# Performance work log

Measured on AMD Instinct MI355X. Metric: run time of the kernel, lower is better.

Reference implementation:

```python
import jax, jax.numpy as jnp
import numpy as np

B, G = 256, 24
N = B * G
D_IN, HEADS, D_HEAD = 128, 8, 64  # out_channels = in_channels//2 = 64, concat=False
EFF = HEADS * D_HEAD
EPS = 1e-5
SCALE = float(np.sqrt(D_HEAD))

def _gelu(x):
    return jax.nn.gelu(x, approximate=False)

def _pff(x, w1, b1, w2, b2):
    # PositionwiseFeedForward, dropout=0 (eval)
    return _gelu(x @ w1.T + b1) @ w2.T + b2

def _graph_norm_global(x, w, b, ms):
    # GraphNorm called without batch -> single graph over all N nodes
    mean = jnp.mean(x, axis=0, keepdims=True)
    out = x - mean * ms
    var = jnp.mean(out * out, axis=0, keepdims=True)
    return w * out / jnp.sqrt(var + EPS) + b

def _graph_norm(x, w, b, ms, batch, nseg):
    cnt = jax.ops.segment_sum(jnp.ones((x.shape[0],), x.dtype), batch, nseg)[:, None]
    mean = jax.ops.segment_sum(x, batch, nseg) / cnt
    out = x - mean[batch] * ms
    var = jax.ops.segment_sum(out * out, batch, nseg) / cnt
    return w * out / jnp.sqrt(var + EPS)[batch] + b

def _segment_softmax(logits, seg, nseg):
    m = jax.ops.segment_max(logits, seg, num_segments=nseg)
    e = jnp.exp(logits - m[seg])
    s = jax.ops.segment_sum(e, seg, num_segments=nseg)
    return e / (s[seg] + 1e-16)

def _attn_conv(x, edge_index, p):
    (nq_w, nq_b, nq_ms, wq, bq, wk, bk, wv, bv,
     no_w, no_b, no_ms, o_w1, o_b1, o_w2, o_b2) = p
    n = x.shape[0]
    xin = x
    xn = _graph_norm_global(x, nq_w, nq_b, nq_ms)
    q = (xn @ wq.T + bq).reshape(n, HEADS, D_HEAD)
    k = (xn @ wk.T + bk).reshape(n, HEADS, D_HEAD)
    v = (xn @ wv.T + bv).reshape(n, HEADS, D_HEAD)
    loops = jnp.arange(n, dtype=edge_index.dtype)  # add_self_loops appends
    src = jnp.concatenate([edge_index[0], loops])
    dst = jnp.concatenate([edge_index[1], loops])
    qk = jnp.sum(q[dst] * k[src], axis=-1) / SCALE          # [E', H]
    alpha = _segment_softmax(qk, dst, n)                     # segment softmax over dst
    aggr = jax.ops.segment_sum(v[src] * alpha[:, :, None], dst, num_segments=n)  # [N,H,Dh]
    aggr = aggr.mean(axis=1)                                 # concat=False: head mean -> [N,64]
    init = xin.reshape(n, D_IN // D_HEAD, D_HEAD).sum(axis=1)  # sum-fold 128 -> 64 residual
    h = aggr + init
    hn = _graph_norm_global(h, no_w, no_b, no_ms)
    return h + _pff(hn, o_w1, o_b1, o_w2, o_b2)


def setup_inputs() -> dict:
    key = jax.random.key(0)
    ks = jax.random.split(key, 12)
    # block-dense edges: fully connected within each set, no self loops
    a = np.arange(G)
    ii, jj = np.meshgrid(a, a, indexing='ij')
    m = ii != jj
    dst_l, src_l = ii[m], jj[m]
    offs = (np.arange(B) * G)[:, None]
    src = (src_l[None, :] + offs).reshape(-1)
    dst = (dst_l[None, :] + offs).reshape(-1)
    edge_index = jnp.asarray(np.stack([src, dst]), dtype=jnp.int64)
    batch = jnp.asarray(np.repeat(np.arange(B), G), dtype=jnp.int64)
    ptr = jnp.asarray(np.arange(B + 1) * G, dtype=jnp.int64)
    x = jax.random.normal(ks[0], (N, D_IN), jnp.float32)
    def lin(k, o, i):
        return jax.random.normal(k, (o, i), jnp.float32) * (1.0 / np.sqrt(i))
    d = dict(x=x, edge_index=edge_index, ptr=ptr, batch=batch)
    d.update(nq_w=jnp.ones((D_IN,)), nq_b=jnp.zeros((D_IN,)), nq_ms=jnp.ones((D_IN,)))
    d.update(wq=lin(ks[1], EFF, D_IN), bq=jnp.zeros((EFF,)),
             wk=lin(ks[2], EFF, D_IN), bk=jnp.zeros((EFF,)),
             wv=lin(ks[3], EFF, D_IN), bv=jnp.zeros((EFF,)))
    d.update(no_w=jnp.ones((D_HEAD,)), no_b=jnp.zeros((D_HEAD,)), no_ms=jnp.ones((D_HEAD,)))
    d.update(o_w1=lin(ks[4], D_HEAD, D_HEAD), o_b1=jnp.zeros((D_HEAD,)),
             o_w2=lin(ks[5], D_HEAD, D_HEAD), o_b2=jnp.zeros((D_HEAD,)))
    d.update(pn_w=jnp.ones((D_HEAD,)), pn_b=jnp.zeros((D_HEAD,)), pn_ms=jnp.ones((D_HEAD,)))
    d.update(p_w1=lin(ks[6], D_HEAD, D_HEAD), p_b1=jnp.zeros((D_HEAD,)),
             p_w2=lin(ks[7], 1, D_HEAD), p_b2=jnp.zeros((1,)))
    return d


def reference(x, edge_index, ptr, batch,
              nq_w, nq_b, nq_ms, wq, bq, wk, bk, wv, bv,
              no_w, no_b, no_ms, o_w1, o_b1, o_w2, o_b2,
              pn_w, pn_b, pn_ms, p_w1, p_b1, p_w2, p_b2):
    nseg = ptr.shape[0] - 1
    h = _attn_conv(x, edge_index,
                   (nq_w, nq_b, nq_ms, wq, bq, wk, bk, wv, bv,
                    no_w, no_b, no_ms, o_w1, o_b1, o_w2, o_b2))   # [N,64]
    hn = _graph_norm(h, pn_w, pn_b, pn_ms, batch, nseg)
    score = _pff(hn, p_w1, p_b1, p_w2, p_b2)                       # [N,1]
    w = _segment_softmax(score[:, 0], batch, nseg)[:, None]        # per-set softmax
    return jax.ops.segment_sum(x * w, batch, num_segments=nseg)    # [B, 128]
```

## Files before the change

kernel.cpp:

```cpp
#include <hip/hip_runtime.h>
#include <stdint.h>


#define N_NODES 6144
#define GSIZE 24
#define NGRAPH 256
#define DIN 128
#define DH 64
#define EFF 512
#define EPSN 1e-5f

typedef __attribute__((ext_vector_type(8))) __bf16 bf16x8;
typedef __attribute__((ext_vector_type(4))) float f32x4;
union U16B { uint4 u; bf16x8 v; unsigned short s[8]; };

__device__ inline unsigned short f2bf(float f){
  unsigned u = __float_as_uint(f);
  u += 0x7fff + ((u>>16)&1);
  return (unsigned short)(u>>16);
}
__device__ inline float gelu_exact(float x){ return 0.5f*x*(1.0f+erff(x*0.70710678118654752f)); }

#define XS    0
#define HS    256
#define HCF   384
#define WT1   393600
#define WT2   397696
#define PWT1  401792
#define FBo   405888
#define WCVT_BYTE  1703936

#define QS3 260

__global__ __launch_bounds__(256)
void k_pre(const float* __restrict__ x,
           const float* __restrict__ o_w1, const float* __restrict__ o_w2,
           const float* __restrict__ p_w1,
           const float* __restrict__ o_b1, const float* __restrict__ o_b2,
           const float* __restrict__ p_b1, const float* __restrict__ p_w2,
           const float* __restrict__ p_b2,
           const float* __restrict__ wq, const float* __restrict__ wk,
           const float* __restrict__ wv,
           float* __restrict__ wsf){
  int t = threadIdx.x;
  int bi = blockIdx.x;
  if(bi < 192){
    int c = t & 127, h = t >> 7;
    float s = 0.f, q = 0.f;
    #pragma unroll
    for(int r = 0; r < 16; ++r){
      float v = x[(size_t)(bi*32 + h + 2*r)*DIN + c];
      s += v; q += v*v;
    }
    __shared__ float sm[256], sm2[256];
    sm[t] = s; sm2[t] = q;
    __syncthreads();
    if(t < 128){
      atomicAdd(&wsf[XS + t],       sm[t] + sm[t+128]);
      atomicAdd(&wsf[XS + 128 + t], sm2[t] + sm2[t+128]);
    }
    return;
  }
  if(bi < 195){
    const float* src; float* dst;
    if(bi == 192){ src = o_w1; dst = wsf + WT1; }
    else if(bi == 193){ src = o_w2; dst = wsf + WT2; }
    else { src = p_w1; dst = wsf + PWT1; }
    for(int p = t; p < DH*DH; p += 256){
      int r = p >> 6, c = p & 63;
      dst[c*DH + r] = src[p];
    }
    if(bi == 192){
      float* fb = wsf + FBo;
      if(t < 64){
        fb[t]       = o_b1[t];
        fb[64 + t]  = o_b2[t];
        fb[128 + t] = p_b1[t];
        fb[192 + t] = p_w2[t];
      }
      if(t == 0) fb[256] = p_b2[0];
    }
    return;
  }
  int j = bi - 195;
  int mat = j >> 2, seg = j & 3;
  const float* src = (mat==0) ? wq : (mat==1) ? wk : wv;
  unsigned short* dst = (unsigned short*)((char*)wsf + WCVT_BYTE)
                        + (size_t)mat*EFF*DIN + seg*16384;
  const float* sp = src + seg*16384;
  for(int e = t*8; e < 16384; e += 2048){
    float4 a = *(const float4*)(sp + e);
    float4 b = *(const float4*)(sp + e + 4);
    U16B o;
    o.s[0]=f2bf(a.x); o.s[1]=f2bf(a.y); o.s[2]=f2bf(a.z); o.s[3]=f2bf(a.w);
    o.s[4]=f2bf(b.x); o.s[5]=f2bf(b.y); o.s[6]=f2bf(b.z); o.s[7]=f2bf(b.w);
    *(uint4*)(dst + e) = o.u;
  }
}

#define LOADW3(nt, W, B) do{ \
  const int mat_ = (nt)>>2, sub_ = (nt)&3; \
  const unsigned short* wp_ = wcvt + (size_t)mat_*EFF*DIN \
      + (size_t)(gh*64 + sub_*16 + m)*DIN + lq*8; \
  W[0] = *(const uint4*)(wp_);      W[1] = *(const uint4*)(wp_ + 32); \
  W[2] = *(const uint4*)(wp_ + 64); W[3] = *(const uint4*)(wp_ + 96); \
  const float* bias_ = (mat_==0) ? bq : (mat_==1) ? bk : bv; \
  B = *(const float4*)(bias_ + gh*64 + sub_*16 + lq*4); \
}while(0)

#define COMPW3(nt, W, B) do{ \
  const int mat_ = (nt)>>2, sub_ = (nt)&3; \
  f32x4 a0_ = {0.f,0.f,0.f,0.f}, a1_ = {0.f,0.f,0.f,0.f}; \
  U16B w8_; \
  w8_.u = W[0]; \
  a0_ = __builtin_amdgcn_mfma_f32_16x16x32_bf16(w8_.v, afr[0][0], a0_, 0, 0, 0); \
  a1_ = __builtin_amdgcn_mfma_f32_16x16x32_bf16(w8_.v, afr[1][0], a1_, 0, 0, 0); \
  w8_.u = W[1]; \
  a0_ = __builtin_amdgcn_mfma_f32_16x16x32_bf16(w8_.v, afr[0][1], a0_, 0, 0, 0); \
  a1_ = __builtin_amdgcn_mfma_f32_16x16x32_bf16(w8_.v, afr[1][1], a1_, 0, 0, 0); \
  w8_.u = W[2]; \
  a0_ = __builtin_amdgcn_mfma_f32_16x16x32_bf16(w8_.v, afr[0][2], a0_, 0, 0, 0); \
  a1_ = __builtin_amdgcn_mfma_f32_16x16x32_bf16(w8_.v, afr[1][2], a1_, 0, 0, 0); \
  w8_.u = W[3]; \
  a0_ = __builtin_amdgcn_mfma_f32_16x16x32_bf16(w8_.v, afr[0][3], a0_, 0, 0, 0); \
  a1_ = __builtin_amdgcn_mfma_f32_16x16x32_bf16(w8_.v, afr[1][3], a1_, 0, 0, 0); \
  float* dst_ = qlds + mat_*(GSIZE*QS3); \
  const int col_ = hh*64 + sub_*16 + lq*4; \
  { float4 o_; o_.x=a0_[0]+B.x; o_.y=a0_[1]+B.y; o_.z=a0_[2]+B.z; o_.w=a0_[3]+B.w; \
    *(float4*)(dst_ + m*QS3 + col_) = o_; } \
  if(m < 8){ float4 o_; o_.x=a1_[0]+B.x; o_.y=a1_[1]+B.y; o_.z=a1_[2]+B.z; o_.w=a1_[3]+B.w; \
    *(float4*)(dst_ + (16+m)*QS3 + col_) = o_; } \
}while(0)

__global__ __launch_bounds__(512)
void k_attn3(const float* __restrict__ x,
             const float* __restrict__ bq, const float* __restrict__ bk,
             const float* __restrict__ bv,
             const float* __restrict__ nq_w, const float* __restrict__ nq_b,
             const float* __restrict__ nq_ms,
             float* __restrict__ ws, float* __restrict__ hcomb){
  __shared__ __align__(16) float qlds[3*GSIZE*QS3];
  float* A1s = qlds;
  float* C1s = qlds + 128;
  float* hv  = qlds + GSIZE*QS3;

  int t = threadIdx.x, b = blockIdx.x;
  int base = (b >> 1)*GSIZE;
  int w = t >> 6, l = t & 63;
  int hh = w >> 1, half = w & 1;
  int gh = (b & 1)*4 + hh;
  const unsigned short* wcvt = (const unsigned short*)((const char*)ws + WCVT_BYTE);

  if(t < 128){
    float s1 = ws[XS + t];
    float q1 = ws[XS + 128 + t];
    float mean = s1 * (1.0f / N_NODES);
    float ex2  = q1 * (1.0f / N_NODES);
    float cm   = mean * nq_ms[t];
    float var  = ex2 - 2.f*cm*mean + cm*cm;
    float rstd = rsqrtf(var + EPSN);
    float a    = nq_w[t] * rstd;
    A1s[t] = a; C1s[t] = nq_b[t] - a*cm;
  }
  __syncthreads();

  int m = l & 15, lq = l >> 4;

  bf16x8 afr[2][4];
  #pragma unroll
  for(int mt = 0; mt < 2; ++mt){
    int row = mt*16 + m; if(row > GSIZE-1) row = GSIZE-1;
    const float* xr = x + (size_t)(base + row)*DIN;
    #pragma unroll
    for(int kk = 0; kk < 4; ++kk){
      int k0 = kk*32 + lq*8;
      float4 a = *(const float4*)(xr + k0);
      float4 b = *(const float4*)(xr + k0 + 4);
      U16B u;
      u.s[0] = f2bf(a.x*A1s[k0+0] + C1s[k0+0]);
      u.s[1] = f2bf(a.y*A1s[k0+1] + C1s[k0+1]);
      u.s[2] = f2bf(a.z*A1s[k0+2] + C1s[k0+2]);
      u.s[3] = f2bf(a.w*A1s[k0+3] + C1s[k0+3]);
      u.s[4] = f2bf(b.x*A1s[k0+4] + C1s[k0+4]);
      u.s[5] = f2bf(b.y*A1s[k0+5] + C1s[k0+5]);
      u.s[6] = f2bf(b.z*A1s[k0+6] + C1s[k0+6]);
      u.s[7] = f2bf(b.w*A1s[k0+7] + C1s[k0+7]);
      afr[mt][kk] = u.v;
    }
  }
  __syncthreads();

  {
    uint4 wA[4], wB[4], wC[4];
    float4 bA, bB, bC;
    int nb = half*6;
    LOADW3(nb+0, wA, bA);  LOADW3(nb+1, wB, bB);
    LOADW3(nb+2, wC, bC);  COMPW3(nb+0, wA, bA);
    LOADW3(nb+3, wA, bA);  COMPW3(nb+1, wB, bB);
    LOADW3(nb+4, wB, bB);  COMPW3(nb+2, wC, bC);
    LOADW3(nb+5, wC, bC);  COMPW3(nb+3, wA, bA);
    COMPW3(nb+4, wB, bB);
    COMPW3(nb+5, wC, bC);
  }
  __syncthreads();

  int r0 = half*12 + 3*(l >> 4), j0 = 3*(l & 7);
  float s00=0.f,s01=0.f,s02=0.f,s10=0.f,s11=0.f,s12=0.f,s20=0.f,s21=0.f,s22=0.f;
  {
    int d8 = (l >> 3) & 1;
    const float* qp = qlds + r0*QS3 + hh*64 + d8*32;
    const float* kp = qlds + GSIZE*QS3 + j0*QS3 + hh*64 + d8*32;
    #pragma unroll
    for(int d4 = 0; d4 < 8; ++d4){
      float4 q0 = *(const float4*)(qp + d4*4);
      float4 q1 = *(const float4*)(qp + QS3 + d4*4);
      float4 q2 = *(const float4*)(qp + 2*QS3 + d4*4);
      float4 k0 = *(const float4*)(kp + d4*4);
      float4 k1 = *(const float4*)(kp + QS3 + d4*4);
      float4 k2 = *(const float4*)(kp + 2*QS3 + d4*4);
      s00 += q0.x*k0.x + q0.y*k0.y + q0.z*k0.z + q0.w*k0.w;
      s01 += q0.x*k1.x + q0.y*k1.y + q0.z*k1.z + q0.w*k1.w;
      s02 += q0.x*k2.x + q0.y*k2.y + q0.z*k2.z + q0.w*k2.w;
      s10 += q1.x*k0.x + q1.y*k0.y + q1.z*k0.z + q1.w*k0.w;
      s11 += q1.x*k1.x + q1.y*k1.y + q1.z*k1.z + q1.w*k1.w;
      s12 += q1.x*k2.x + q1.y*k2.y + q1.z*k2.z + q1.w*k2.w;
      s20 += q2.x*k0.x + q2.y*k0.y + q2.z*k0.z + q2.w*k0.w;
      s21 += q2.x*k1.x + q2.y*k1.y + q2.z*k1.z + q2.w*k1.w;
      s22 += q2.x*k2.x + q2.y*k2.y + q2.z*k2.z + q2.w*k2.w;
    }
    s00 += __shfl_xor(s00, 8); s01 += __shfl_xor(s01, 8); s02 += __shfl_xor(s02, 8);
    s10 += __shfl_xor(s10, 8); s11 += __shfl_xor(s11, 8); s12 += __shfl_xor(s12, 8);
    s20 += __shfl_xor(s20, 8); s21 += __shfl_xor(s21, 8); s22 += __shfl_xor(s22, 8);
  }
  __syncthreads();

  {
    float a0, a1, a2, m0, su, inv;
    float* STb = qlds + hh*64;
    a0 = s00*0.125f; a1 = s01*0.125f; a2 = s02*0.125f;
    m0 = fmaxf(fmaxf(a0, a1), a2);
    #pragma unroll
    for(int o = 1; o < 8; o <<= 1) m0 = fmaxf(m0, __shfl_xor(m0, o, 8));
    a0 = __expf(a0-m0); a1 = __expf(a1-m0); a2 = __expf(a2-m0);
    su = a0 + a1 + a2;
    #pragma unroll
    for(int o = 1; o < 8; o <<= 1) su += __shfl_xor(su, o, 8);
    inv = 1.0f/(su + 1e-16f);
    STb[(j0+0)*QS3 + r0] = a0*inv; STb[(j0+1)*QS3 + r0] = a1*inv; STb[(j0+2)*QS3 + r0] = a2*inv;
    a0 = s10*0.125f; a1 = s11*0.125f; a2 = s12*0.125f;
    m0 = fmaxf(fmaxf(a0, a1), a2);
    #pragma unroll
    for(int o = 1; o < 8; o <<= 1) m0 = fmaxf(m0, __shfl_xor(m0, o, 8));
    a0 = __expf(a0-m0); a1 = __expf(a1-m0); a2 = __expf(a2-m0);
    su = a0 + a1 + a2;
    #pragma unroll
    for(int o = 1; o < 8; o <<= 1) su += __shfl_xor(su, o, 8);
    inv = 1.0f/(su + 1e-16f);
    STb[(j0+0)*QS3 + r0+1] = a0*inv; STb[(j0+1)*QS3 + r0+1] = a1*inv; STb[(j0+2)*QS3 + r0+1] = a2*inv;
    a0 = s20*0.125f; a1 = s21*0.125f; a2 = s22*0.125f;
    m0 = fmaxf(fmaxf(a0, a1), a2);
    #pragma unroll
    for(int o = 1; o < 8; o <<= 1) m0 = fmaxf(m0, __shfl_xor(m0, o, 8));
    a0 = __expf(a0-m0); a1 = __expf(a1-m0); a2 = __expf(a2-m0);
    su = a0 + a1 + a2;
    #pragma unroll
    for(int o = 1; o < 8; o <<= 1) su += __shfl_xor(su, o, 8);
    inv = 1.0f/(su + 1e-16f);
    STb[(j0+0)*QS3 + r0+2] = a0*inv; STb[(j0+1)*QS3 + r0+2] = a1*inv; STb[(j0+2)*QS3 + r0+2] = a2*inv;
  }
  for(int i = t; i < GSIZE*DH; i += 512) hv[i] = 0.f;
  __syncthreads();

  {
    float o12[12];
    #pragma unroll
    for(int r = 0; r < 12; ++r) o12[r] = 0.f;
    const float* vp  = qlds + 2*GSIZE*QS3 + hh*64 + l;
    const float* STb = qlds + hh*64;
    int rb = half*12;
    #pragma unroll
    for(int j = 0; j < GSIZE; ++j){
      float v = vp[j*QS3];
      #pragma unroll
      for(int rq = 0; rq < 3; ++rq){
        float4 p4 = *(const float4*)(STb + j*QS3 + rb + rq*4);
        o12[rq*4+0] = fmaf(p4.x, v, o12[rq*4+0]);
        o12[rq*4+1] = fmaf(p4.y, v, o12[rq*4+1]);
        o12[rq*4+2] = fmaf(p4.z, v, o12[rq*4+2]);
        o12[rq*4+3] = fmaf(p4.w, v, o12[rq*4+3]);
      }
    }
    #pragma unroll
    for(int r = 0; r < 12; ++r) atomicAdd(&hv[(rb + r)*DH + l], o12[r]);
  }
  __syncthreads();

  #pragma unroll
  for(int sl = 0; sl < 3; ++sl){
    int idx = t + sl*512;
    int r = idx >> 6, d = idx & 63;
    atomicAdd(&hcomb[(size_t)(base + r)*DH + d], hv[r*DH + d]*0.125f);
  }
}

__global__ __launch_bounds__(256)
void k_hfix(const float* __restrict__ x, float* __restrict__ ws,
            float* __restrict__ hcomb){
  __shared__ float redA[256], redB[256];
  int t = threadIdx.x, b = blockIdx.x;
  int d = t & 63, rg = t >> 6;
  int r0 = b*32 + rg*8;
  float s1 = 0.f, s2 = 0.f;
  #pragma unroll
  for(int k = 0; k < 8; ++k){
    int r = r0 + k;
    const float* xr = x + (size_t)r*DIN;
    float v = hcomb[(size_t)r*DH + d] + xr[d] + xr[64 + d];
    hcomb[(size_t)r*DH + d] = v;
    s1 += v; s2 += v*v;
  }
  redA[t] = s1; redB[t] = s2;
  __syncthreads();
  if(t < 64){
    float a1 = redA[t] + redA[t+64] + redA[t+128] + redA[t+192];
    float a2 = redB[t] + redB[t+64] + redB[t+128] + redB[t+192];
    atomicAdd(&ws[HS + t],      a1);
    atomicAdd(&ws[HS + 64 + t], a2);
  }
}

__global__ __launch_bounds__(512)
void k_final(const float* __restrict__ x,
             const float* __restrict__ hbuf, const float* __restrict__ ws,
             const float* __restrict__ no_w, const float* __restrict__ no_b,
             const float* __restrict__ no_ms,
             const float* __restrict__ pn_w, const float* __restrict__ pn_b,
             const float* __restrict__ pn_ms,
             float* __restrict__ out){
  __shared__ __align__(16) float W1[4096];
  __shared__ __align__(16) float W2[4096];
  __shared__ __align__(16) float PW1[4096];
  __shared__ __align__(16) float fbs[260];
  __shared__ __align__(16) float hs[GSIZE][68];
  __shared__ __align__(16) float hn[GSIZE][68];
  __shared__ __align__(16) float ts[GSIZE][68];
  __shared__ float A2s[DH], C2s[DH];
  __shared__ float a3[DH], c3[DH];
  __shared__ float scores[GSIZE], wsm[GSIZE];

  int t = threadIdx.x;
  int base = blockIdx.x * GSIZE;
  int c = t & 63, i0 = t >> 6;

  {
    const float4* s1 = (const float4*)(ws + WT1);
    const float4* s2 = (const float4*)(ws + WT2);
    const float4* s3 = (const float4*)(ws + PWT1);
    #pragma unroll
    for(int it = 0; it < 2; ++it){
      int i = t + it*512;
      ((float4*)W1)[i]  = s1[i];
      ((float4*)W2)[i]  = s2[i];
      ((float4*)PW1)[i] = s3[i];
    }
    if(t < 257) fbs[t] = ws[FBo + t];
    if(t < DH){
      float a1 = ws[HS + t];
      float a2 = ws[HS + 64 + t];
      float mean = a1 * (1.0f / N_NODES);
      float ex2  = a2 * (1.0f / N_NODES);
      float cm   = mean * no_ms[t];
      float var  = ex2 - 2.f*cm*mean + cm*cm;
      float rstd = rsqrtf(var + EPSN);
      float a    = no_w[t] * rstd;
      A2s[t] = a; C2s[t] = no_b[t] - a*cm;
    }
  }
  __syncthreads();
  {
    float a2 = A2s[c];
    float c2 = C2s[c];
    #pragma unroll
    for(int r = 0; r < 3; ++r){
      int i = i0 + 8*r;
      float hvv = hbuf[(size_t)(base + i)*DH + c];
      hs[i][c] = hvv;
      hn[i][c] = a2*hvv + c2;
    }
  }
  __syncthreads();

  {
    float acc[3];
    #pragma unroll
    for(int r = 0; r < 3; ++r) acc[r] = fbs[c];
    #pragma unroll 16
    for(int k = 0; k < DH; ++k){
      float w = W1[k*DH + c];
      #pragma unroll
      for(int r = 0; r < 3; ++r) acc[r] = fmaf(hn[i0 + 8*r][k], w, acc[r]);
    }
    #pragma unroll
    for(int r = 0; r < 3; ++r) ts[i0 + 8*r][c] = gelu_exact(acc[r]);
  }
  __syncthreads();

  {
    float acc[3];
    #pragma unroll
    for(int r = 0; r < 3; ++r) acc[r] = fbs[64 + c];
    #pragma unroll 16
    for(int k = 0; k < DH; ++k){
      float w = W2[k*DH + c];
      #pragma unroll
      for(int r = 0; r < 3; ++r) acc[r] = fmaf(ts[i0 + 8*r][k], w, acc[r]);
    }
    #pragma unroll
    for(int r = 0; r < 3; ++r) hs[i0 + 8*r][c] += acc[r];
  }
  __syncthreads();

  if(t < DH){
    float s1 = 0.f, s2 = 0.f;
    #pragma unroll
    for(int i = 0; i < GSIZE; i++){ float v = hs[i][t]; s1 += v; s2 += v*v; }
    float mean = s1 * (1.0f / GSIZE);
    float ex2  = s2 * (1.0f / GSIZE);
    float cm   = mean * pn_ms[t];
    float var  = ex2 - 2.f*cm*mean + cm*cm;
    float rstd = rsqrtf(var + EPSN);
    float a    = pn_w[t] * rstd;
    a3[t] = a; c3[t] = pn_b[t] - a*cm;
  }
  __syncthreads();

  {
    float acc[3];
    #pragma unroll
    for(int r = 0; r < 3; ++r) acc[r] = fbs[128 + c];
    #pragma unroll 16
    for(int k = 0; k < DH; ++k){
      float w  = PW1[k*DH + c];
      float ak = a3[k], ck = c3[k];
      #pragma unroll
      for(int r = 0; r < 3; ++r){
        float hnv = fmaf(ak, hs[i0 + 8*r][k], ck);
        acc[r] = fmaf(hnv, w, acc[r]);
      }
    }
    #pragma unroll
    for(int r = 0; r < 3; ++r) ts[i0 + 8*r][c] = gelu_exact(acc[r]);
  }
  __syncthreads();

  if(t < GSIZE){
    const float4* tp = (const float4*)ts[t];
    const float4* wp = (const float4*)(fbs + 192);
    float s = fbs[256];
    #pragma unroll
    for(int q = 0; q < 16; ++q){
      float4 a = tp[q], b = wp[q];
      s += a.x*b.x + a.y*b.y + a.z*b.z + a.w*b.w;
    }
    scores[t] = s;
  }
  __syncthreads();
  if(t < GSIZE){
    float mx = -1e30f;
    #pragma unroll
    for(int j = 0; j < GSIZE; j++) mx = fmaxf(mx, scores[j]);
    float sum = 0.f;
    #pragma unroll
    for(int j = 0; j < GSIZE; j++) sum += __expf(scores[j] - mx);
    wsm[t] = __expf(scores[t] - mx) / (sum + 1e-16f);
  }
  __syncthreads();
  if(t < DIN){
    float s = 0.f;
    #pragma unroll 8
    for(int i = 0; i < GSIZE; i++) s += wsm[i] * x[(size_t)(base+i)*DIN + t];
    out[(size_t)blockIdx.x*DIN + t] = s;
  }
}

extern "C" void kernel_launch(void* const* d_in, const int* in_sizes, int n_in,
                              void* d_out, int out_size, void* d_ws, size_t ws_size,
                              hipStream_t stream){
  (void)in_sizes; (void)n_in; (void)out_size; (void)ws_size;
  const float* x    = (const float*)d_in[0];
  const float* nq_w = (const float*)d_in[4];
  const float* nq_b = (const float*)d_in[5];
  const float* nq_ms= (const float*)d_in[6];
  const float* wq   = (const float*)d_in[7];
  const float* bq   = (const float*)d_in[8];
  const float* wk   = (const float*)d_in[9];
  const float* bk   = (const float*)d_in[10];
  const float* wv   = (const float*)d_in[11];
  const float* bv   = (const float*)d_in[12];
  const float* no_w = (const float*)d_in[13];
  const float* no_b = (const float*)d_in[14];
  const float* no_ms= (const float*)d_in[15];
  const float* o_w1 = (const float*)d_in[16];
  const float* o_b1 = (const float*)d_in[17];
  const float* o_w2 = (const float*)d_in[18];
  const float* o_b2 = (const float*)d_in[19];
  const float* pn_w = (const float*)d_in[20];
  const float* pn_b = (const float*)d_in[21];
  const float* pn_ms= (const float*)d_in[22];
  const float* p_w1 = (const float*)d_in[23];
  const float* p_b1 = (const float*)d_in[24];
  const float* p_w2 = (const float*)d_in[25];
  const float* p_b2 = (const float*)d_in[26];

  float* ws    = (float*)d_ws;
  float* hcomb = ws + HCF;

  hipMemsetAsync(d_ws, 0, (size_t)(384 + N_NODES*DH)*sizeof(float), stream);
  k_pre<<<207, 256, 0, stream>>>(x, o_w1, o_w2, p_w1, o_b1, o_b2, p_b1, p_w2, p_b2,
                                 wq, wk, wv, ws);
  k_attn3<<<512, 512, 0, stream>>>(x, bq, bk, bv, nq_w, nq_b, nq_ms, ws, hcomb);
  k_hfix<<<192, 256, 0, stream>>>(x, ws, hcomb);
  k_final<<<NGRAPH, 512, 0, stream>>>(x, hcomb, ws, no_w, no_b, no_ms,
                                      pn_w, pn_b, pn_ms, (float*)d_out);
}
```

Measured before the change: 179.4 us.

## Split attention kernel to one head per block and keep probabilities in registers

```diff
diff --git a/kernel.cpp b/kernel.cpp
--- a/kernel.cpp
+++ b/kernel.cpp
@@ -30,7 +30,7 @@
 #define FBo   405888
 #define WCVT_BYTE  1703936
 
-#define QS3 260
+#define QS1 68
 
 __global__ __launch_bounds__(256)
 void k_pre(const float* __restrict__ x,
@@ -98,17 +98,17 @@
   }
 }
 
-#define LOADW3(nt, W, B) do{ \
+#define LOADW1(nt, W, B) do{ \
   const int mat_ = (nt)>>2, sub_ = (nt)&3; \
   const unsigned short* wp_ = wcvt + (size_t)mat_*EFF*DIN \
-      + (size_t)(gh*64 + sub_*16 + m)*DIN + lq*8; \
+      + (size_t)(h*64 + sub_*16 + m)*DIN + lq*8; \
   W[0] = *(const uint4*)(wp_);      W[1] = *(const uint4*)(wp_ + 32); \
   W[2] = *(const uint4*)(wp_ + 64); W[3] = *(const uint4*)(wp_ + 96); \
   const float* bias_ = (mat_==0) ? bq : (mat_==1) ? bk : bv; \
-  B = *(const float4*)(bias_ + gh*64 + sub_*16 + lq*4); \
+  B = *(const float4*)(bias_ + h*64 + sub_*16 + lq*4); \
 }while(0)
 
-#define COMPW3(nt, W, B) do{ \
+#define COMPW1(nt, W, B) do{ \
   const int mat_ = (nt)>>2, sub_ = (nt)&3; \
   f32x4 a0_ = {0.f,0.f,0.f,0.f}, a1_ = {0.f,0.f,0.f,0.f}; \
   U16B w8_; \
@@ -124,31 +124,27 @@
   w8_.u = W[3]; \
   a0_ = __builtin_amdgcn_mfma_f32_16x16x32_bf16(w8_.v, afr[0][3], a0_, 0, 0, 0); \
   a1_ = __builtin_amdgcn_mfma_f32_16x16x32_bf16(w8_.v, afr[1][3], a1_, 0, 0, 0); \
-  float* dst_ = qlds + mat_*(GSIZE*QS3); \
-  const int col_ = hh*64 + sub_*16 + lq*4; \
+  float* dst_ = qlds + mat_*(GSIZE*QS1); \
+  const int col_ = sub_*16 + lq*4; \
   { float4 o_; o_.x=a0_[0]+B.x; o_.y=a0_[1]+B.y; o_.z=a0_[2]+B.z; o_.w=a0_[3]+B.w; \
-    *(float4*)(dst_ + m*QS3 + col_) = o_; } \
+    *(float4*)(dst_ + m*QS1 + col_) = o_; } \
   if(m < 8){ float4 o_; o_.x=a1_[0]+B.x; o_.y=a1_[1]+B.y; o_.z=a1_[2]+B.z; o_.w=a1_[3]+B.w; \
-    *(float4*)(dst_ + (16+m)*QS3 + col_) = o_; } \
+    *(float4*)(dst_ + (16+m)*QS1 + col_) = o_; } \
 }while(0)
 
-__global__ __launch_bounds__(512)
-void k_attn3(const float* __restrict__ x,
+__global__ __launch_bounds__(256)
+void k_attn4(const float* __restrict__ x,
              const float* __restrict__ bq, const float* __restrict__ bk,
              const float* __restrict__ bv,
              const float* __restrict__ nq_w, const float* __restrict__ nq_b,
              const float* __restrict__ nq_ms,
              float* __restrict__ ws, float* __restrict__ hcomb){
-  __shared__ __align__(16) float qlds[3*GSIZE*QS3];
-  float* A1s = qlds;
-  float* C1s = qlds + 128;
-  float* hv  = qlds + GSIZE*QS3;
+  __shared__ __align__(16) float qlds[3*GSIZE*QS1];
+  __shared__ float A1s[DIN], C1s[DIN];
 
   int t = threadIdx.x, b = blockIdx.x;
-  int base = (b >> 1)*GSIZE;
+  int g = b >> 3, h = b & 7, base = g*GSIZE;
   int w = t >> 6, l = t & 63;
-  int hh = w >> 1, half = w & 1;
-  int gh = (b & 1)*4 + hh;
   const unsigned short* wcvt = (const unsigned short*)((const char*)ws + WCVT_BYTE);
 
   if(t < 128){
@@ -175,49 +171,46 @@
     for(int kk = 0; kk < 4; ++kk){
       int k0 = kk*32 + lq*8;
       float4 a = *(const float4*)(xr + k0);
-      float4 b = *(const float4*)(xr + k0 + 4);
+      float4 bb = *(const float4*)(xr + k0 + 4);
       U16B u;
       u.s[0] = f2bf(a.x*A1s[k0+0] + C1s[k0+0]);
       u.s[1] = f2bf(a.y*A1s[k0+1] + C1s[k0+1]);
       u.s[2] = f2bf(a.z*A1s[k0+2] + C1s[k0+2]);
       u.s[3] = f2bf(a.w*A1s[k0+3] + C1s[k0+3]);
-      u.s[4] = f2bf(b.x*A1s[k0+4] + C1s[k0+4]);
-      u.s[5] = f2bf(b.y*A1s[k0+5] + C1s[k0+5]);
-      u.s[6] = f2bf(b.z*A1s[k0+6] + C1s[k0+6]);
-      u.s[7] = f2bf(b.w*A1s[k0+7] + C1s[k0+7]);
+      u.s[4] = f2bf(bb.x*A1s[k0+4] + C1s[k0+4]);
+      u.s[5] = f2bf(bb.y*A1s[k0+5] + C1s[k0+5]);
+      u.s[6] = f2bf(bb.z*A1s[k0+6] + C1s[k0+6]);
+      u.s[7] = f2bf(bb.w*A1s[k0+7] + C1s[k0+7]);
       afr[mt][kk] = u.v;
     }
   }
-  __syncthreads();
-
-  {
-    uint4 wA[4], wB[4], wC[4];
-    float4 bA, bB, bC;
-    int nb = half*6;
-    LOADW3(nb+0, wA, bA);  LOADW3(nb+1, wB, bB);
-    LOADW3(nb+2, wC, bC);  COMPW3(nb+0, wA, bA);
-    LOADW3(nb+3, wA, bA);  COMPW3(nb+1, wB, bB);
-    LOADW3(nb+4, wB, bB);  COMPW3(nb+2, wC, bC);
-    LOADW3(nb+5, wC, bC);  COMPW3(nb+3, wA, bA);
-    COMPW3(nb+4, wB, bB);
-    COMPW3(nb+5, wC, bC);
-  }
-  __syncthreads();
-
-  int r0 = half*12 + 3*(l >> 4), j0 = 3*(l & 7);
-  float s00=0.f,s01=0.f,s02=0.f,s10=0.f,s11=0.f,s12=0.f,s20=0.f,s21=0.f,s22=0.f;
-  {
-    int d8 = (l >> 3) & 1;
-    const float* qp = qlds + r0*QS3 + hh*64 + d8*32;
-    const float* kp = qlds + GSIZE*QS3 + j0*QS3 + hh*64 + d8*32;
-    #pragma unroll
-    for(int d4 = 0; d4 < 8; ++d4){
+
+  {
+    uint4 wA[4], wB[4];
+    float4 bA, bB;
+    int nb = w*3;
+    LOADW1(nb+0, wA, bA);  LOADW1(nb+1, wB, bB);
+    COMPW1(nb+0, wA, bA);  LOADW1(nb+2, wA, bA);
+    COMPW1(nb+1, wB, bB);
+    COMPW1(nb+2, wA, bA);
+  }
+  __syncthreads();
+
+  float pr[3][3];
+  {
+    int sl = l & 15, dq = l >> 4;
+    int r0 = w*6 + (sl >> 3)*3, j0 = (sl & 7)*3;
+    const float* qp = qlds + r0*QS1 + dq*16;
+    const float* kp = qlds + GSIZE*QS1 + j0*QS1 + dq*16;
+    float s00=0.f,s01=0.f,s02=0.f,s10=0.f,s11=0.f,s12=0.f,s20=0.f,s21=0.f,s22=0.f;
+    #pragma unroll
+    for(int d4 = 0; d4 < 4; ++d4){
       float4 q0 = *(const float4*)(qp + d4*4);
-      float4 q1 = *(const float4*)(qp + QS3 + d4*4);
-      float4 q2 = *(const float4*)(qp + 2*QS3 + d4*4);
+      float4 q1 = *(const float4*)(qp + QS1 + d4*4);
+      float4 q2 = *(const float4*)(qp + 2*QS1 + d4*4);
       float4 k0 = *(const float4*)(kp + d4*4);
-      float4 k1 = *(const float4*)(kp + QS3 + d4*4);
-      float4 k2 = *(const float4*)(kp + 2*QS3 + d4*4);
+      float4 k1 = *(const float4*)(kp + QS1 + d4*4);
+      float4 k2 = *(const float4*)(kp + 2*QS1 + d4*4);
       s00 += q0.x*k0.x + q0.y*k0.y + q0.z*k0.z + q0.w*k0.w;
       s01 += q0.x*k1.x + q0.y*k1.y + q0.z*k1.z + q0.w*k1.w;
       s02 += q0.x*k2.x + q0.y*k2.y + q0.z*k2.z + q0.w*k2.w;
@@ -228,15 +221,14 @@
       s21 += q2.x*k1.x + q2.y*k1.y + q2.z*k1.z + q2.w*k1.w;
       s22 += q2.x*k2.x + q2.y*k2.y + q2.z*k2.z + q2.w*k2.w;
     }
-    s00 += __shfl_xor(s00, 8); s01 += __shfl_xor(s01, 8); s02 += __shfl_xor(s02, 8);
-    s10 += __shfl_xor(s10, 8); s11 += __shfl_xor(s11, 8); s12 += __shfl_xor(s12, 8);
-    s20 += __shfl_xor(s20, 8); s21 += __shfl_xor(s21, 8); s22 += __shfl_xor(s22, 8);
-  }
-  __syncthreads();
-
-  {
+    s00 += __shfl_xor(s00, 16); s01 += __shfl_xor(s01, 16); s02 += __shfl_xor(s02, 16);
+    s10 += __shfl_xor(s10, 16); s11 += __shfl_xor(s11, 16); s12 += __shfl_xor(s12, 16);
+    s20 += __shfl_xor(s20, 16); s21 += __shfl_xor(s21, 16); s22 += __shfl_xor(s22, 16);
+    s00 += __shfl_xor(s00, 32); s01 += __shfl_xor(s01, 32); s02 += __shfl_xor(s02, 32);
+    s10 += __shfl_xor(s10, 32); s11 += __shfl_xor(s11, 32); s12 += __shfl_xor(s12, 32);
+    s20 += __shfl_xor(s20, 32); s21 += __shfl_xor(s21, 32); s22 += __shfl_xor(s22, 32);
+
     float a0, a1, a2, m0, su, inv;
-    float* STb = qlds + hh*64;
     a0 = s00*0.125f; a1 = s01*0.125f; a2 = s02*0.125f;
     m0 = fmaxf(fmaxf(a0, a1), a2);
     #pragma unroll
@@ -246,7 +238,7 @@
     #pragma unroll
     for(int o = 1; o < 8; o <<= 1) su += __shfl_xor(su, o, 8);
     inv = 1.0f/(su + 1e-16f);
-    STb[(j0+0)*QS3 + r0] = a0*inv; STb[(j0+1)*QS3 + r0] = a1*inv; STb[(j0+2)*QS3 + r0] = a2*inv;
+    pr[0][0] = a0*inv; pr[0][1] = a1*inv; pr[0][2] = a2*inv;
     a0 = s10*0.125f; a1 = s11*0.125f; a2 = s12*0.125f;
     m0 = fmaxf(fmaxf(a0, a1), a2);
     #pragma unroll
@@ -256,7 +248,7 @@
     #pragma unroll
     for(int o = 1; o < 8; o <<= 1) su += __shfl_xor(su, o, 8);
     inv = 1.0f/(su + 1e-16f);
-    STb[(j0+0)*QS3 + r0+1] = a0*inv; STb[(j0+1)*QS3 + r0+1] = a1*inv; STb[(j0+2)*QS3 + r0+1] = a2*inv;
+    pr[1][0] = a0*inv; pr[1][1] = a1*inv; pr[1][2] = a2*inv;
     a0 = s20*0.125f; a1 = s21*0.125f; a2 = s22*0.125f;
     m0 = fmaxf(fmaxf(a0, a1), a2);
     #pragma unroll
@@ -266,40 +258,34 @@
     #pragma unroll
     for(int o = 1; o < 8; o <<= 1) su += __shfl_xor(su, o, 8);
     inv = 1.0f/(su + 1e-16f);
-    STb[(j0+0)*QS3 + r0+2] = a0*inv; STb[(j0+1)*QS3 + r0+2] = a1*inv; STb[(j0+2)*QS3 + r0+2] = a2*inv;
-  }
-  for(int i = t; i < GSIZE*DH; i += 512) hv[i] = 0.f;
-  __syncthreads();
-
-  {
-    float o12[12];
-    #pragma unroll
-    for(int r = 0; r < 12; ++r) o12[r] = 0.f;
-    const float* vp  = qlds + 2*GSIZE*QS3 + hh*64 + l;
-    const float* STb = qlds + hh*64;
-    int rb = half*12;
+    pr[2][0] = a0*inv; pr[2][1] = a1*inv; pr[2][2] = a2*inv;
+  }
+
+  {
+    float o6[6];
+    #pragma unroll
+    for(int r = 0; r < 6; ++r) o6[r] = 0.f;
+    const float* vp = qlds + 2*GSIZE*QS1 + l;
     #pragma unroll
     for(int j = 0; j < GSIZE; ++j){
-      float v = vp[j*QS3];
+      float v = vp[j*QS1];
+      const int jg = j/3, jj = j%3;
       #pragma unroll
-      for(int rq = 0; rq < 3; ++rq){
-        float4 p4 = *(const float4*)(STb + j*QS3 + rb + rq*4);
-        o12[rq*4+0] = fmaf(p4.x, v, o12[rq*4+0]);
-        o12[rq*4+1] = fmaf(p4.y, v, o12[rq*4+1]);
-        o12[rq*4+2] = fmaf(p4.z, v, o12[rq*4+2]);
-        o12[rq*4+3] = fmaf(p4.w, v, o12[rq*4+3]);
+      for(int a = 0; a < 2; ++a){
+        #pragma unroll
+        for(int rr = 0; rr < 3; ++rr){
+          float pv = __uint_as_float(
+              __builtin_amdgcn_readlane(__float_as_uint(pr[rr][jj]), a*8 + jg));
+          o6[a*3+rr] = fmaf(pv, v, o6[a*3+rr]);
+        }
       }
     }
     #pragma unroll
-    for(int r = 0; r < 12; ++r) atomicAdd(&hv[(rb + r)*DH + l], o12[r]);
-  }
-  __syncthreads();
-
-  #pragma unroll
-  for(int sl = 0; sl < 3; ++sl){
-    int idx = t + sl*512;
-    int r = idx >> 6, d = idx & 63;
-    atomicAdd(&hcomb[(size_t)(base + r)*DH + d], hv[r*DH + d]*0.125f);
+    for(int a = 0; a < 2; ++a)
+      #pragma unroll
+      for(int rr = 0; rr < 3; ++rr)
+        atomicAdd(&hcomb[(size_t)(base + w*6 + a*3 + rr)*DH + l],
+                  o6[a*3+rr]*0.125f);
   }
 }
 
@@ -518,7 +504,7 @@
   hipMemsetAsync(d_ws, 0, (size_t)(384 + N_NODES*DH)*sizeof(float), stream);
   k_pre<<<207, 256, 0, stream>>>(x, o_w1, o_w2, p_w1, o_b1, o_b2, p_b1, p_w2, p_b2,
                                  wq, wk, wv, ws);
-  k_attn3<<<512, 512, 0, stream>>>(x, bq, bk, bv, nq_w, nq_b, nq_ms, ws, hcomb);
+  k_attn4<<<2048, 256, 0, stream>>>(x, bq, bk, bv, nq_w, nq_b, nq_ms, ws, hcomb);
   k_hfix<<<192, 256, 0, stream>>>(x, ws, hcomb);
   k_final<<<NGRAPH, 512, 0, stream>>>(x, hcomb, ws, no_w, no_b, no_ms,
                                       pn_w, pn_b, pn_ms, (float*)d_out);
```

Measured after the change: 161.5 us, median of 2. 1.11x faster.
